# Performance work log

Measured on AMD Instinct MI355X. Metric: run time of the kernel, lower is better.

Reference implementation:

```python
import jax, jax.numpy as jnp
import numpy as np
from jax import lax

FS, DW, CIN, COUT, NCLS, BATCH = 128, 8, 64, 256, 2, 512
K1, S1 = FS // 4, FS // 8          # 32, 16
L = FS * DW                        # 1024
T = (L - K1) // S1 + 1             # 63 SNN timesteps
BN_EPS = 1e-5


@jax.custom_vjp
def spike(u):
    """Heaviside spike on (v - threshold); surrogate grad exp(-|u|) (tau_grad=scale_grad=1)."""
    return (u >= 0).astype(u.dtype)

def _spike_fwd(u):
    return (u >= 0).astype(u.dtype), u

def _spike_bwd(u, g):
    return (g * jnp.exp(-jnp.abs(u)),)

spike.defvjp(_spike_fwd, _spike_bwd)


def cuba(x, threshold, current_decay, voltage_decay):
    """CUBA LIF scan. x: [N,C,T] -> binary spikes [N,C,T].
    i[t] = (1-cd)*i[t-1] + x[t]; v[t] = (1-vd)*v[t-1] + i[t]; s = v>=theta; v *= (1-s)."""
    cd, vd = 1.0 - current_decay, 1.0 - voltage_decay
    xs = jnp.moveaxis(x, -1, 0)  # [T,N,C]
    zero = jnp.zeros(x.shape[:-1], x.dtype)

    def step(carry, xt):
        i, v = carry
        i = cd * i + xt
        v = vd * v + i
        s = spike(v - threshold)
        v = v * (1.0 - s)
        return (i, v), s

    _, s = lax.scan(step, (zero, zero), xs)
    return jnp.moveaxis(s, 0, -1)


def conv1d(x, w, b, stride, pad):
    y = lax.conv_general_dilated(x, w, (stride,), [(pad, pad)],
                                 dimension_numbers=('NCH', 'OIH', 'NCH'))
    return y + b[None, :, None]


def bn(x, g, b, m, v):
    scale = g / jnp.sqrt(v + BN_EPS)
    return (x - m[None, :, None]) * scale[None, :, None] + b[None, :, None]


def setup_inputs() -> dict:
    key = jax.random.key(0)
    ks = jax.random.split(key, 12)
    return {
        'x':       jax.random.normal(ks[0], (BATCH, CIN, L), jnp.float32),
        'conv1_w': jax.random.normal(ks[1], (COUT, CIN, K1), jnp.float32) * 0.05,
        'conv1_b': jax.random.normal(ks[2], (COUT,), jnp.float32) * 0.05,
        'bn1_g':   jax.random.uniform(ks[3], (COUT,), jnp.float32, 0.5, 1.5),
        'bn1_b':   jax.random.normal(ks[4], (COUT,), jnp.float32) * 0.1,
        'bn1_m':   jax.random.normal(ks[5], (COUT,), jnp.float32) * 0.1,
        'bn1_v':   jax.random.uniform(ks[6], (COUT,), jnp.float32, 0.5, 1.5),
        'conv2_w': jax.random.normal(ks[7], (COUT, COUT, 3), jnp.float32) * 0.05,
        'conv2_b': jax.random.normal(ks[8], (COUT,), jnp.float32) * 0.05,
        'bn2_g':   jax.random.uniform(ks[9], (COUT,), jnp.float32, 0.5, 1.5),
        'bn2_b':   jax.random.normal(ks[10], (COUT,), jnp.float32) * 0.1,
        'bn2_m':   jax.random.normal(ks[11], (COUT,), jnp.float32) * 0.1,
        'bn2_v':   jax.random.uniform(jax.random.fold_in(key, 100), (COUT,), jnp.float32, 0.5, 1.5),
        'w1':      jax.random.normal(jax.random.fold_in(key, 101), (COUT, COUT), jnp.float32) * 0.1,
        'w2':      jax.random.normal(jax.random.fold_in(key, 102), (NCLS, COUT), jnp.float32) * 0.1,
    }


def reference(x, conv1_w, conv1_b, bn1_g, bn1_b, bn1_m, bn1_v,
              conv2_w, conv2_b, bn2_g, bn2_b, bn2_m, bn2_v, w1, w2):
    # CNN frontend (eval mode: BN uses running stats, dropout is identity)
    z = bn(conv1d(x, conv1_w, conv1_b, S1, 0), bn1_g, bn1_b, bn1_m, bn1_v)   # [N,COUT,T]
    z = bn(conv1d(z, conv2_w, conv2_b, 1, 1), bn2_g, bn2_b, bn2_m, bn2_v)    # [N,COUT,T]
    # CUBA Input encoder block: threshold=0.3, current_decay=0.9, voltage_decay=0.9
    z = cuba(z, 0.3, 0.9, 0.9)
    # CUBA Dense blocks (bias-free synapse per timestep + LIF): threshold=0.1, cd=1, vd=0.1
    z = cuba(jnp.einsum('oc,nct->not', w1, z), 0.1, 1.0, 0.1)
    z = cuba(jnp.einsum('oc,nct->not', w2, z), 0.1, 1.0, 0.1)
    return z  # binary spike trains [N, n_classes, T]
```

## Files before the change

### kernel.cpp

```cpp
#include <hip/hip_runtime.h>
#include <cstdint>
#include <cstddef>


typedef _Float16 half8 __attribute__((ext_vector_type(8)));
typedef float floatx4 __attribute__((ext_vector_type(4)));

__device__ __forceinline__ void split_f32(float v, _Float16& hi, _Float16& lo) {
    _Float16 h = (_Float16)v;
    hi = h;
    lo = (_Float16)((v - (float)h) * 2048.0f);
}

typedef const __attribute__((address_space(1))) unsigned int* gas_ptr;
typedef __attribute__((address_space(3))) unsigned int* las_ptr;
__device__ __forceinline__ void lds_dma16(const void* g, void* l) {
    __builtin_amdgcn_global_load_lds((gas_ptr)g, (las_ptr)l, 16, 0, 0);
}

__global__ __launch_bounds__(256) void prep_kernel(
    const float* __restrict__ c1w, const float* __restrict__ c1b,
    const float* __restrict__ g1,  const float* __restrict__ b1,
    const float* __restrict__ m1,  const float* __restrict__ v1,
    const float* __restrict__ c2w, const float* __restrict__ c2b,
    const float* __restrict__ g2,  const float* __restrict__ b2,
    const float* __restrict__ m2,  const float* __restrict__ v2,
    const float* __restrict__ w1,
    _Float16* __restrict__ w1h, _Float16* __restrict__ w1l,
    _Float16* __restrict__ w2h, _Float16* __restrict__ w2l,
    _Float16* __restrict__ wdh, _Float16* __restrict__ wdl,
    float* __restrict__ ab1, float* __restrict__ ab2)
{
    const int id = blockIdx.x * 256 + threadIdx.x;
    if (id < 256) {
        float a1 = g1[id] / sqrtf(v1[id] + 1e-5f);
        ab1[id]       = a1;
        ab1[256 + id] = (c1b[id] - m1[id]) * a1 + b1[id];
        float a2 = g2[id] / sqrtf(v2[id] + 1e-5f);
        ab2[id]       = a2;
        ab2[256 + id] = (c2b[id] - m2[id]) * a2 + b2[id];
    }
    split_f32(w1[id], wdh[id], wdl[id]);
    for (int idx = id; idx < 256 * 2048; idx += 65536)
        split_f32(c1w[idx], w1h[idx], w1l[idx]);
    for (int idx = id; idx < 256 * 768; idx += 65536) {
        const int o  = idx / 768;
        const int r  = idx - o * 768;
        const int dt = r >> 8;
        const int c  = r & 255;
        split_f32(c2w[o * 768 + c * 3 + dt], w2h[idx], w2l[idx]);
    }
}

__global__ __launch_bounds__(256, 2) void conv1_mfma(
    const float* __restrict__ x,
    const _Float16* __restrict__ w1h, const _Float16* __restrict__ w1l,
    const float* __restrict__ ab,
    _Float16* __restrict__ z1h, _Float16* __restrict__ z1l)
{
    __shared__ _Float16 Ah[2][4][128][8];
    __shared__ _Float16 Al[2][4][128][8];
    __shared__ _Float16 Bh[2][4][128][8];
    __shared__ _Float16 Bl[2][4][128][8];

    const int tid = threadIdx.x;
    const int bm = blockIdx.x, bn = blockIdx.y;
    const int lr = tid & 127;
    const int h  = tid >> 7;

    const int am = bm * 128 + lr;
    const int an = am / 63, at = am - an * 63;
    const float* arow = x + (size_t)an * 65536 + at * 16 + h * 16;

    const int lane = tid & 63;
    const int wv   = tid >> 6;
    const int mw   = wv & 1, nw = wv >> 1;
    const int quad = lane >> 4;
    const int l15  = lane & 15;

    const int q0 = wv >> 1;
    const int rh = (wv & 1) * 64;
    const _Float16* bh_g = w1h + (size_t)(bn * 128 + rh + lane) * 2048;
    const _Float16* bl_g = w1l + (size_t)(bn * 128 + rh + lane) * 2048;

    floatx4 accA[4][4] = {};
    floatx4 accB[4][4] = {};

    union U { _Float16 hf[8]; int4 v; };
    float va[16];

    {
        *(float4*)&va[0]  = *(const float4*)(arow);
        *(float4*)&va[4]  = *(const float4*)(arow + 4);
        *(float4*)&va[8]  = *(const float4*)(arow + 8);
        *(float4*)&va[12] = *(const float4*)(arow + 12);
        lds_dma16(bh_g + q0 * 8,       &Bh[0][q0    ][rh][0]);
        lds_dma16(bh_g + (q0 + 2) * 8, &Bh[0][q0 + 2][rh][0]);
        lds_dma16(bl_g + q0 * 8,       &Bl[0][q0    ][rh][0]);
        lds_dma16(bl_g + (q0 + 2) * 8, &Bl[0][q0 + 2][rh][0]);
        U c0h, c0l, c1h, c1l;
#pragma unroll
        for (int j = 0; j < 8; ++j) split_f32(va[j],     c0h.hf[j], c0l.hf[j]);
#pragma unroll
        for (int j = 0; j < 8; ++j) split_f32(va[8 + j], c1h.hf[j], c1l.hf[j]);
        *(int4*)&Ah[0][2*h  ][lr][0] = c0h.v;
        *(int4*)&Ah[0][2*h+1][lr][0] = c1h.v;
        *(int4*)&Al[0][2*h  ][lr][0] = c0l.v;
        *(int4*)&Al[0][2*h+1][lr][0] = c1l.v;
        __syncthreads();
    }

    int cur = 0;
    for (int it = 0; it < 64; ++it) {
        const int nxt = cur ^ 1;
        const bool pf = (it < 63);

        if (pf) {
            const float* ap = arow + (it + 1) * 1024;
            *(float4*)&va[0]  = *(const float4*)(ap);
            *(float4*)&va[4]  = *(const float4*)(ap + 4);
            *(float4*)&va[8]  = *(const float4*)(ap + 8);
            *(float4*)&va[12] = *(const float4*)(ap + 12);
            const int ko = (it + 1) * 32;
            lds_dma16(bh_g + ko + q0 * 8,       &Bh[nxt][q0    ][rh][0]);
            lds_dma16(bh_g + ko + (q0 + 2) * 8, &Bh[nxt][q0 + 2][rh][0]);
            lds_dma16(bl_g + ko + q0 * 8,       &Bl[nxt][q0    ][rh][0]);
            lds_dma16(bl_g + ko + (q0 + 2) * 8, &Bl[nxt][q0 + 2][rh][0]);
        }

        half8 fah[4], fal[4], fbh[4], fbl[4];
#pragma unroll
        for (int t = 0; t < 4; ++t) {
            fah[t] = *(const half8*)&Ah[cur][quad][mw*64 + t*16 + l15][0];
            fal[t] = *(const half8*)&Al[cur][quad][mw*64 + t*16 + l15][0];
            fbh[t] = *(const half8*)&Bh[cur][quad][nw*64 + t*16 + l15][0];
            fbl[t] = *(const half8*)&Bl[cur][quad][nw*64 + t*16 + l15][0];
        }
#pragma unroll
        for (int ti = 0; ti < 4; ++ti)
#pragma unroll
            for (int tj = 0; tj < 4; ++tj) {
                accA[ti][tj] = __builtin_amdgcn_mfma_f32_16x16x32_f16(fah[ti], fbh[tj], accA[ti][tj], 0, 0, 0);
                accB[ti][tj] = __builtin_amdgcn_mfma_f32_16x16x32_f16(fah[ti], fbl[tj], accB[ti][tj], 0, 0, 0);
                accB[ti][tj] = __builtin_amdgcn_mfma_f32_16x16x32_f16(fal[ti], fbh[tj], accB[ti][tj], 0, 0, 0);
            }

        if (pf) {
            U c0h, c0l, c1h, c1l;
#pragma unroll
            for (int j = 0; j < 8; ++j) split_f32(va[j],     c0h.hf[j], c0l.hf[j]);
#pragma unroll
            for (int j = 0; j < 8; ++j) split_f32(va[8 + j], c1h.hf[j], c1l.hf[j]);
            *(int4*)&Ah[nxt][2*h  ][lr][0] = c0h.v;
            *(int4*)&Ah[nxt][2*h+1][lr][0] = c1h.v;
            *(int4*)&Al[nxt][2*h  ][lr][0] = c0l.v;
            *(int4*)&Al[nxt][2*h+1][lr][0] = c1l.v;
        }
        __syncthreads();
        cur = nxt;
    }

#pragma unroll
    for (int tj = 0; tj < 4; ++tj) {
        const int o = bn*128 + nw*64 + tj*16 + l15;
        const float alpha = ab[o], beta = ab[256 + o];
#pragma unroll
        for (int ti = 0; ti < 4; ++ti) {
            const int m0 = bm*128 + mw*64 + ti*16 + quad*4;
#pragma unroll
            for (int r = 0; r < 4; ++r) {
                float c = accA[ti][tj][r] + accB[ti][tj][r] * (1.0f/2048.0f);
                float z = c * alpha + beta;
                _Float16 zh, zl;
                split_f32(z, zh, zl);
                const size_t off = (size_t)(m0 + r) * 256 + o;
                z1h[off] = zh;
                z1l[off] = zl;
            }
        }
    }
}

__global__ __launch_bounds__(256, 2) void conv2_mfma(
    const _Float16* __restrict__ z1h, const _Float16* __restrict__ z1l,
    const _Float16* __restrict__ w2h, const _Float16* __restrict__ w2l,
    const float* __restrict__ ab, float* __restrict__ z2)
{
    __shared__ _Float16 Ah[2][4][128][8];
    __shared__ _Float16 Al[2][4][128][8];
    __shared__ _Float16 Bh[2][4][128][8];
    __shared__ _Float16 Bl[2][4][128][8];

    const int tid = threadIdx.x;
    const int bm = blockIdx.x, bn = blockIdx.y;
    const int lr = tid & 127;
    const int h  = tid >> 7;

    const int am = bm * 128 + lr;
    const int an = am / 63, at = am - an * 63;
    const _Float16* abase_h = z1h + (size_t)an * 16128;
    const _Float16* abase_l = z1l + (size_t)an * 16128;

    const int lane = tid & 63;
    const int wv   = tid >> 6;
    const int mw   = wv & 1, nw = wv >> 1;
    const int quad = lane >> 4;
    const int l15  = lane & 15;

    const int q0 = wv >> 1;
    const int rh = (wv & 1) * 64;
    const _Float16* bh_g = w2h + (size_t)(bn * 128 + rh + lane) * 768;
    const _Float16* bl_g = w2l + (size_t)(bn * 128 + rh + lane) * 768;

    floatx4 accA[4][4] = {};
    floatx4 accB[4][4] = {};

    const int4 z4 = {0, 0, 0, 0};
    int4 a0h, a1h, a0l, a1l;

    auto loadA = [&](int it, int4& r0h, int4& r1h, int4& r0l, int4& r1l) {
        const int kap0 = it * 32;
        const int dt   = kap0 >> 8;
        const int c0   = kap0 & 255;
        const int trow = at + dt - 1;
        const bool valid = (trow >= 0) && (trow < 63);
        const _Float16* aph = abase_h + trow * 256 + c0 + h * 16;
        const _Float16* apl = abase_l + trow * 256 + c0 + h * 16;
        r0h = valid ? *(const int4*)(aph)     : z4;
        r1h = valid ? *(const int4*)(aph + 8) : z4;
        r0l = valid ? *(const int4*)(apl)     : z4;
        r1l = valid ? *(const int4*)(apl + 8) : z4;
    };

    {
        loadA(0, a0h, a1h, a0l, a1l);
        lds_dma16(bh_g + q0 * 8,       &Bh[0][q0    ][rh][0]);
        lds_dma16(bh_g + (q0 + 2) * 8, &Bh[0][q0 + 2][rh][0]);
        lds_dma16(bl_g + q0 * 8,       &Bl[0][q0    ][rh][0]);
        lds_dma16(bl_g + (q0 + 2) * 8, &Bl[0][q0 + 2][rh][0]);
        *(int4*)&Ah[0][2*h  ][lr][0] = a0h;
        *(int4*)&Ah[0][2*h+1][lr][0] = a1h;
        *(int4*)&Al[0][2*h  ][lr][0] = a0l;
        *(int4*)&Al[0][2*h+1][lr][0] = a1l;
        __syncthreads();
    }

    int cur = 0;
    for (int it = 0; it < 24; ++it) {
        const int nxt = cur ^ 1;
        const bool pf = (it < 23);

        if (pf) {
            loadA(it + 1, a0h, a1h, a0l, a1l);
            const int ko = (it + 1) * 32;
            lds_dma16(bh_g + ko + q0 * 8,       &Bh[nxt][q0    ][rh][0]);
            lds_dma16(bh_g + ko + (q0 + 2) * 8, &Bh[nxt][q0 + 2][rh][0]);
            lds_dma16(bl_g + ko + q0 * 8,       &Bl[nxt][q0    ][rh][0]);
            lds_dma16(bl_g + ko + (q0 + 2) * 8, &Bl[nxt][q0 + 2][rh][0]);
        }

        half8 fah[4], fal[4], fbh[4], fbl[4];
#pragma unroll
        for (int t = 0; t < 4; ++t) {
            fah[t] = *(const half8*)&Ah[cur][quad][mw*64 + t*16 + l15][0];
            fal[t] = *(const half8*)&Al[cur][quad][mw*64 + t*16 + l15][0];
            fbh[t] = *(const half8*)&Bh[cur][quad][nw*64 + t*16 + l15][0];
            fbl[t] = *(const half8*)&Bl[cur][quad][nw*64 + t*16 + l15][0];
        }
#pragma unroll
        for (int ti = 0; ti < 4; ++ti)
#pragma unroll
            for (int tj = 0; tj < 4; ++tj) {
                accA[ti][tj] = __builtin_amdgcn_mfma_f32_16x16x32_f16(fah[ti], fbh[tj], accA[ti][tj], 0, 0, 0);
                accB[ti][tj] = __builtin_amdgcn_mfma_f32_16x16x32_f16(fah[ti], fbl[tj], accB[ti][tj], 0, 0, 0);
                accB[ti][tj] = __builtin_amdgcn_mfma_f32_16x16x32_f16(fal[ti], fbh[tj], accB[ti][tj], 0, 0, 0);
            }

        if (pf) {
            *(int4*)&Ah[nxt][2*h  ][lr][0] = a0h;
            *(int4*)&Ah[nxt][2*h+1][lr][0] = a1h;
            *(int4*)&Al[nxt][2*h  ][lr][0] = a0l;
            *(int4*)&Al[nxt][2*h+1][lr][0] = a1l;
        }
        __syncthreads();
        cur = nxt;
    }

#pragma unroll
    for (int tj = 0; tj < 4; ++tj) {
        const int o = bn*128 + nw*64 + tj*16 + l15;
        const float alpha = ab[o], beta = ab[256 + o];
#pragma unroll
        for (int ti = 0; ti < 4; ++ti) {
            const int m0 = bm*128 + mw*64 + ti*16 + quad*4;
#pragma unroll
            for (int r = 0; r < 4; ++r) {
                float c = accA[ti][tj][r] + accB[ti][tj][r] * (1.0f/2048.0f);
                z2[(size_t)(m0 + r) * 256 + o] = c * alpha + beta;
            }
        }
    }
}

__global__ __launch_bounds__(256) void cuba1_kernel(
    const float* __restrict__ z2, _Float16* __restrict__ s1)
{
    const int n   = blockIdx.x;
    const int tid = threadIdx.x;
    const float* zrow = z2 + (size_t)n * 16128 + tid;
    _Float16*    srow = s1 + (size_t)n * 16128 + tid;
    float cur = 0.f, vol = 0.f;
    for (int t = 0; t < 63; ++t) {
        float xv = zrow[(size_t)t * 256];
        cur = 0.1f * cur + xv;
        vol = 0.1f * vol + cur;
        bool sp = (vol - 0.3f) >= 0.f;
        srow[(size_t)t * 256] = sp ? (_Float16)1.0f : (_Float16)0.0f;
        if (sp) vol = 0.f;
    }
}

__global__ __launch_bounds__(256, 2) void dense1_mfma(
    const _Float16* __restrict__ s1,
    const _Float16* __restrict__ wdh, const _Float16* __restrict__ wdl,
    float* __restrict__ y1)
{
    __shared__ _Float16 As[2][4][128][8];
    __shared__ _Float16 Bh[2][4][128][8];
    __shared__ _Float16 Bl[2][4][128][8];

    const int tid = threadIdx.x;
    const int bm = blockIdx.x, bn = blockIdx.y;

    const int lane = tid & 63;
    const int wv   = tid >> 6;
    const int mw   = wv & 1, nw = wv >> 1;
    const int quad = lane >> 4;
    const int l15  = lane & 15;

    const int q0 = wv >> 1;
    const int rh = (wv & 1) * 64;
    const _Float16* a_g  = s1  + (size_t)(bm * 128 + rh + lane) * 256;
    const _Float16* bh_g = wdh + (size_t)(bn * 128 + rh + lane) * 256;
    const _Float16* bl_g = wdl + (size_t)(bn * 128 + rh + lane) * 256;

    floatx4 accA[4][4] = {};
    floatx4 accB[4][4] = {};

    {
        lds_dma16(a_g  + q0 * 8,       &As[0][q0    ][rh][0]);
        lds_dma16(a_g  + (q0 + 2) * 8, &As[0][q0 + 2][rh][0]);
        lds_dma16(bh_g + q0 * 8,       &Bh[0][q0    ][rh][0]);
        lds_dma16(bh_g + (q0 + 2) * 8, &Bh[0][q0 + 2][rh][0]);
        lds_dma16(bl_g + q0 * 8,       &Bl[0][q0    ][rh][0]);
        lds_dma16(bl_g + (q0 + 2) * 8, &Bl[0][q0 + 2][rh][0]);
        __syncthreads();
    }

    int cur = 0;
    for (int it = 0; it < 8; ++it) {
        const int nxt = cur ^ 1;
        const bool pf = (it < 7);

        if (pf) {
            const int ko = (it + 1) * 32;
            lds_dma16(a_g  + ko + q0 * 8,       &As[nxt][q0    ][rh][0]);
            lds_dma16(a_g  + ko + (q0 + 2) * 8, &As[nxt][q0 + 2][rh][0]);
            lds_dma16(bh_g + ko + q0 * 8,       &Bh[nxt][q0    ][rh][0]);
            lds_dma16(bh_g + ko + (q0 + 2) * 8, &Bh[nxt][q0 + 2][rh][0]);
            lds_dma16(bl_g + ko + q0 * 8,       &Bl[nxt][q0    ][rh][0]);
            lds_dma16(bl_g + ko + (q0 + 2) * 8, &Bl[nxt][q0 + 2][rh][0]);
        }

        half8 fa[4], fbh[4], fbl[4];
#pragma unroll
        for (int t = 0; t < 4; ++t) {
            fa[t]  = *(const half8*)&As[cur][quad][mw*64 + t*16 + l15][0];
            fbh[t] = *(const half8*)&Bh[cur][quad][nw*64 + t*16 + l15][0];
            fbl[t] = *(const half8*)&Bl[cur][quad][nw*64 + t*16 + l15][0];
        }
#pragma unroll
        for (int ti = 0; ti < 4; ++ti)
#pragma unroll
            for (int tj = 0; tj < 4; ++tj) {
                accA[ti][tj] = __builtin_amdgcn_mfma_f32_16x16x32_f16(fa[ti], fbh[tj], accA[ti][tj], 0, 0, 0);
                accB[ti][tj] = __builtin_amdgcn_mfma_f32_16x16x32_f16(fa[ti], fbl[tj], accB[ti][tj], 0, 0, 0);
            }

        __syncthreads();
        cur = nxt;
    }

#pragma unroll
    for (int tj = 0; tj < 4; ++tj) {
        const int o = bn*128 + nw*64 + tj*16 + l15;
#pragma unroll
        for (int ti = 0; ti < 4; ++ti) {
            const int m0 = bm*128 + mw*64 + ti*16 + quad*4;
#pragma unroll
            for (int r = 0; r < 4; ++r)
                y1[(size_t)(m0 + r) * 256 + o] =
                    accA[ti][tj][r] + accB[ti][tj][r] * (1.0f/2048.0f);
        }
    }
}

__global__ __launch_bounds__(256) void snn_tail(
    const float* __restrict__ y1, const float* __restrict__ w2,
    float* __restrict__ out)
{
    __shared__ unsigned long long M2[256];
    __shared__ float Y[2 * 63];
    const int n   = blockIdx.x;
    const int tid = threadIdx.x;

    {
        const float* yrow = y1 + (size_t)n * 16128 + tid;
        float v = 0.f;
        unsigned long long mask2 = 0ull;
        for (int t = 0; t < 63; ++t) {
            float yv = yrow[(size_t)t * 256];
            v = 0.9f * v + yv;
            if ((v - 0.1f) >= 0.f) { mask2 |= (1ull << t); v = 0.f; }
        }
        M2[tid] = mask2;
    }
    __syncthreads();

    if (tid < 126) {
        const int cls = tid / 63;
        const int t   = tid - cls * 63;
        const float* wrow = w2 + cls * 256;
        float acc = 0.f;
#pragma unroll 4
        for (int o = 0; o < 256; ++o)
            acc += ((M2[o] >> t) & 1ull) ? wrow[o] : 0.f;
        Y[cls * 63 + t] = acc;
    }
    __syncthreads();
    if (tid < 2) {
        float v = 0.f;
        float* orow = out + (size_t)n * 126 + tid * 63;
        for (int t = 0; t < 63; ++t) {
            v = 0.9f * v + Y[tid * 63 + t];
            float u = v - 0.1f;
            float s = (u >= 0.f) ? 1.f : 0.f;
            orow[t] = s;
            v = (u >= 0.f) ? 0.f : v;
        }
    }
}

extern "C" void kernel_launch(void* const* d_in, const int* in_sizes, int n_in,
                              void* d_out, int out_size, void* d_ws, size_t ws_size,
                              hipStream_t stream)
{
    const float* x    = (const float*)d_in[0];
    const float* c1w  = (const float*)d_in[1];
    const float* c1b  = (const float*)d_in[2];
    const float* g1   = (const float*)d_in[3];
    const float* b1   = (const float*)d_in[4];
    const float* m1   = (const float*)d_in[5];
    const float* v1   = (const float*)d_in[6];
    const float* c2w  = (const float*)d_in[7];
    const float* c2b  = (const float*)d_in[8];
    const float* g2   = (const float*)d_in[9];
    const float* b2   = (const float*)d_in[10];
    const float* m2   = (const float*)d_in[11];
    const float* v2   = (const float*)d_in[12];
    const float* w1   = (const float*)d_in[13];
    const float* w2   = (const float*)d_in[14];
    float* out = (float*)d_out;

    float* ws = (float*)d_ws;
    float*    zA  = ws;
    _Float16* z1h = (_Float16*)zA;
    _Float16* z1l = (_Float16*)(zA + 4128768);
    float*    y1  = zA;
    float*    z2  = zA + 8257536;
    _Float16* s1  = (_Float16*)(z2 + 8257536);
    float*    wsp = z2 + 8257536 + 4128768;
    _Float16* w1h = (_Float16*)wsp;
    _Float16* w1l = (_Float16*)(wsp + 262144);
    _Float16* w2h = (_Float16*)(wsp + 2*262144);
    _Float16* w2l = (_Float16*)(wsp + 2*262144 + 98304);
    _Float16* wdh = (_Float16*)(wsp + 2*262144 + 2*98304);
    _Float16* wdl = (_Float16*)(wsp + 2*262144 + 2*98304 + 32768);
    float*    ab1 = wsp + 2*262144 + 2*98304 + 2*32768;
    float*    ab2 = ab1 + 512;

    prep_kernel<<<256, 256, 0, stream>>>(c1w, c1b, g1, b1, m1, v1,
                                         c2w, c2b, g2, b2, m2, v2,
                                         w1, w1h, w1l, w2h, w2l, wdh, wdl,
                                         ab1, ab2);
    conv1_mfma<<<dim3(252, 2), 256, 0, stream>>>(x, w1h, w1l, ab1, z1h, z1l);
    conv2_mfma<<<dim3(252, 2), 256, 0, stream>>>(z1h, z1l, w2h, w2l, ab2, z2);
    cuba1_kernel<<<512, 256, 0, stream>>>(z2, s1);
    dense1_mfma<<<dim3(252, 2), 256, 0, stream>>>(s1, wdh, wdl, y1);
    snn_tail<<<512, 256, 0, stream>>>(y1, w2, out);
}
```

Before: 449.7 us.

## Deepen prefetch pipelines with partial vmcnt barriers in conv and dense GEMMs

```diff
diff --git a/kernel.cpp b/kernel.cpp
--- a/kernel.cpp
+++ b/kernel.cpp
@@ -17,6 +17,8 @@
 __device__ __forceinline__ void lds_dma16(const void* g, void* l) {
     __builtin_amdgcn_global_load_lds((gas_ptr)g, (las_ptr)l, 16, 0, 0);
 }
+
+#define BARRIER_VM(N) asm volatile("s_waitcnt vmcnt(" #N ") lgkmcnt(0)\n\ts_barrier" ::: "memory")
 
 __global__ __launch_bounds__(256) void prep_kernel(
     const float* __restrict__ c1w, const float* __restrict__ c1b,
@@ -87,46 +89,53 @@
     floatx4 accB[4][4] = {};
 
     union U { _Float16 hf[8]; int4 v; };
-    float va[16];
+    float va0[16], va1[16];
 
     {
-        *(float4*)&va[0]  = *(const float4*)(arow);
-        *(float4*)&va[4]  = *(const float4*)(arow + 4);
-        *(float4*)&va[8]  = *(const float4*)(arow + 8);
-        *(float4*)&va[12] = *(const float4*)(arow + 12);
         lds_dma16(bh_g + q0 * 8,       &Bh[0][q0    ][rh][0]);
         lds_dma16(bh_g + (q0 + 2) * 8, &Bh[0][q0 + 2][rh][0]);
         lds_dma16(bl_g + q0 * 8,       &Bl[0][q0    ][rh][0]);
         lds_dma16(bl_g + (q0 + 2) * 8, &Bl[0][q0 + 2][rh][0]);
+        __builtin_amdgcn_sched_barrier(0);
+        *(float4*)&va0[0]  = *(const float4*)(arow);
+        *(float4*)&va0[4]  = *(const float4*)(arow + 4);
+        *(float4*)&va0[8]  = *(const float4*)(arow + 8);
+        *(float4*)&va0[12] = *(const float4*)(arow + 12);
+        const float* ap1 = arow + 1024;
+        *(float4*)&va1[0]  = *(const float4*)(ap1);
+        *(float4*)&va1[4]  = *(const float4*)(ap1 + 4);
+        *(float4*)&va1[8]  = *(const float4*)(ap1 + 8);
+        *(float4*)&va1[12] = *(const float4*)(ap1 + 12);
         U c0h, c0l, c1h, c1l;
 #pragma unroll
-        for (int j = 0; j < 8; ++j) split_f32(va[j],     c0h.hf[j], c0l.hf[j]);
-#pragma unroll
-        for (int j = 0; j < 8; ++j) split_f32(va[8 + j], c1h.hf[j], c1l.hf[j]);
+        for (int j = 0; j < 8; ++j) split_f32(va0[j],     c0h.hf[j], c0l.hf[j]);
+#pragma unroll
+        for (int j = 0; j < 8; ++j) split_f32(va0[8 + j], c1h.hf[j], c1l.hf[j]);
         *(int4*)&Ah[0][2*h  ][lr][0] = c0h.v;
         *(int4*)&Ah[0][2*h+1][lr][0] = c1h.v;
         *(int4*)&Al[0][2*h  ][lr][0] = c0l.v;
         *(int4*)&Al[0][2*h+1][lr][0] = c1l.v;
-        __syncthreads();
-    }
-
-    int cur = 0;
-    for (int it = 0; it < 64; ++it) {
+        BARRIER_VM(4);
+    }
+
+    auto body = [&](int it, float (&vaC)[16], float (&vaN)[16], int cur) {
         const int nxt = cur ^ 1;
-        const bool pf = (it < 63);
-
-        if (pf) {
-            const float* ap = arow + (it + 1) * 1024;
-            *(float4*)&va[0]  = *(const float4*)(ap);
-            *(float4*)&va[4]  = *(const float4*)(ap + 4);
-            *(float4*)&va[8]  = *(const float4*)(ap + 8);
-            *(float4*)&va[12] = *(const float4*)(ap + 12);
+        if (it + 1 < 64) {
             const int ko = (it + 1) * 32;
             lds_dma16(bh_g + ko + q0 * 8,       &Bh[nxt][q0    ][rh][0]);
             lds_dma16(bh_g + ko + (q0 + 2) * 8, &Bh[nxt][q0 + 2][rh][0]);
             lds_dma16(bl_g + ko + q0 * 8,       &Bl[nxt][q0    ][rh][0]);
             lds_dma16(bl_g + ko + (q0 + 2) * 8, &Bl[nxt][q0 + 2][rh][0]);
         }
+        __builtin_amdgcn_sched_barrier(0);
+        if (it + 2 < 64) {
+            const float* ap = arow + (it + 2) * 1024;
+            *(float4*)&vaC[0]  = *(const float4*)(ap);
+            *(float4*)&vaC[4]  = *(const float4*)(ap + 4);
+            *(float4*)&vaC[8]  = *(const float4*)(ap + 8);
+            *(float4*)&vaC[12] = *(const float4*)(ap + 12);
+        }
+        __builtin_amdgcn_sched_barrier(0);
 
         half8 fah[4], fal[4], fbh[4], fbl[4];
 #pragma unroll
@@ -145,19 +154,24 @@
                 accB[ti][tj] = __builtin_amdgcn_mfma_f32_16x16x32_f16(fal[ti], fbh[tj], accB[ti][tj], 0, 0, 0);
             }
 
-        if (pf) {
+        if (it + 1 < 64) {
             U c0h, c0l, c1h, c1l;
 #pragma unroll
-            for (int j = 0; j < 8; ++j) split_f32(va[j],     c0h.hf[j], c0l.hf[j]);
-#pragma unroll
-            for (int j = 0; j < 8; ++j) split_f32(va[8 + j], c1h.hf[j], c1l.hf[j]);
+            for (int j = 0; j < 8; ++j) split_f32(vaN[j],     c0h.hf[j], c0l.hf[j]);
+#pragma unroll
+            for (int j = 0; j < 8; ++j) split_f32(vaN[8 + j], c1h.hf[j], c1l.hf[j]);
             *(int4*)&Ah[nxt][2*h  ][lr][0] = c0h.v;
             *(int4*)&Ah[nxt][2*h+1][lr][0] = c1h.v;
             *(int4*)&Al[nxt][2*h  ][lr][0] = c0l.v;
             *(int4*)&Al[nxt][2*h+1][lr][0] = c1l.v;
         }
-        __syncthreads();
-        cur = nxt;
+        if (it + 2 < 64)      { BARRIER_VM(4); }
+        else if (it + 1 < 64) { BARRIER_VM(0); }
+    };
+
+    for (int it = 0; it < 64; it += 2) {
+        body(it,     va0, va1, 0);
+        body(it + 1, va1, va0, 1);
     }
 
 #pragma unroll
@@ -216,48 +230,51 @@
     floatx4 accB[4][4] = {};
 
     const int4 z4 = {0, 0, 0, 0};
-    int4 a0h, a1h, a0l, a1l;
-
-    auto loadA = [&](int it, int4& r0h, int4& r1h, int4& r0l, int4& r1l) {
+    int4 wA0[4], wA1[4];
+    bool v0, v1;
+
+    auto issueA = [&](int it, int4 (&w)[4], bool& valid) {
         const int kap0 = it * 32;
         const int dt   = kap0 >> 8;
         const int c0   = kap0 & 255;
         const int trow = at + dt - 1;
-        const bool valid = (trow >= 0) && (trow < 63);
-        const _Float16* aph = abase_h + trow * 256 + c0 + h * 16;
-        const _Float16* apl = abase_l + trow * 256 + c0 + h * 16;
-        r0h = valid ? *(const int4*)(aph)     : z4;
-        r1h = valid ? *(const int4*)(aph + 8) : z4;
-        r0l = valid ? *(const int4*)(apl)     : z4;
-        r1l = valid ? *(const int4*)(apl + 8) : z4;
+        valid = (trow >= 0) && (trow < 63);
+        const int trc  = trow < 0 ? 0 : (trow > 62 ? 62 : trow);
+        const _Float16* aph = abase_h + trc * 256 + c0 + h * 16;
+        const _Float16* apl = abase_l + trc * 256 + c0 + h * 16;
+        w[0] = *(const int4*)(aph);
+        w[1] = *(const int4*)(aph + 8);
+        w[2] = *(const int4*)(apl);
+        w[3] = *(const int4*)(apl + 8);
     };
 
     {
-        loadA(0, a0h, a1h, a0l, a1l);
         lds_dma16(bh_g + q0 * 8,       &Bh[0][q0    ][rh][0]);
         lds_dma16(bh_g + (q0 + 2) * 8, &Bh[0][q0 + 2][rh][0]);
         lds_dma16(bl_g + q0 * 8,       &Bl[0][q0    ][rh][0]);
         lds_dma16(bl_g + (q0 + 2) * 8, &Bl[0][q0 + 2][rh][0]);
-        *(int4*)&Ah[0][2*h  ][lr][0] = a0h;
-        *(int4*)&Ah[0][2*h+1][lr][0] = a1h;
-        *(int4*)&Al[0][2*h  ][lr][0] = a0l;
-        *(int4*)&Al[0][2*h+1][lr][0] = a1l;
-        __syncthreads();
-    }
-
-    int cur = 0;
-    for (int it = 0; it < 24; ++it) {
+        __builtin_amdgcn_sched_barrier(0);
+        issueA(0, wA0, v0);
+        issueA(1, wA1, v1);
+        *(int4*)&Ah[0][2*h  ][lr][0] = v0 ? wA0[0] : z4;
+        *(int4*)&Ah[0][2*h+1][lr][0] = v0 ? wA0[1] : z4;
+        *(int4*)&Al[0][2*h  ][lr][0] = v0 ? wA0[2] : z4;
+        *(int4*)&Al[0][2*h+1][lr][0] = v0 ? wA0[3] : z4;
+        BARRIER_VM(4);
+    }
+
+    auto body = [&](int it, int4 (&wC)[4], bool& vC, int4 (&wN)[4], bool& vN, int cur) {
         const int nxt = cur ^ 1;
-        const bool pf = (it < 23);
-
-        if (pf) {
-            loadA(it + 1, a0h, a1h, a0l, a1l);
+        if (it + 1 < 24) {
             const int ko = (it + 1) * 32;
             lds_dma16(bh_g + ko + q0 * 8,       &Bh[nxt][q0    ][rh][0]);
             lds_dma16(bh_g + ko + (q0 + 2) * 8, &Bh[nxt][q0 + 2][rh][0]);
             lds_dma16(bl_g + ko + q0 * 8,       &Bl[nxt][q0    ][rh][0]);
             lds_dma16(bl_g + ko + (q0 + 2) * 8, &Bl[nxt][q0 + 2][rh][0]);
         }
+        __builtin_amdgcn_sched_barrier(0);
+        if (it + 2 < 24) issueA(it + 2, wC, vC);
+        __builtin_amdgcn_sched_barrier(0);
 
         half8 fah[4], fal[4], fbh[4], fbl[4];
 #pragma unroll
@@ -276,14 +293,19 @@
                 accB[ti][tj] = __builtin_amdgcn_mfma_f32_16x16x32_f16(fal[ti], fbh[tj], accB[ti][tj], 0, 0, 0);
             }
 
-        if (pf) {
-            *(int4*)&Ah[nxt][2*h  ][lr][0] = a0h;
-            *(int4*)&Ah[nxt][2*h+1][lr][0] = a1h;
-            *(int4*)&Al[nxt][2*h  ][lr][0] = a0l;
-            *(int4*)&Al[nxt][2*h+1][lr][0] = a1l;
-        }
-        __syncthreads();
-        cur = nxt;
+        if (it + 1 < 24) {
+            *(int4*)&Ah[nxt][2*h  ][lr][0] = vN ? wN[0] : z4;
+            *(int4*)&Ah[nxt][2*h+1][lr][0] = vN ? wN[1] : z4;
+            *(int4*)&Al[nxt][2*h  ][lr][0] = vN ? wN[2] : z4;
+            *(int4*)&Al[nxt][2*h+1][lr][0] = vN ? wN[3] : z4;
+        }
+        if (it + 2 < 24)      { BARRIER_VM(4); }
+        else if (it + 1 < 24) { BARRIER_VM(0); }
+    };
+
+    for (int it = 0; it < 24; it += 2) {
+        body(it,     wA0, v0, wA1, v1, 0);
+        body(it + 1, wA1, v1, wA0, v0, 1);
     }
 
 #pragma unroll
@@ -310,13 +332,19 @@
     const float* zrow = z2 + (size_t)n * 16128 + tid;
     _Float16*    srow = s1 + (size_t)n * 16128 + tid;
     float cur = 0.f, vol = 0.f;
-    for (int t = 0; t < 63; ++t) {
-        float xv = zrow[(size_t)t * 256];
-        cur = 0.1f * cur + xv;
-        vol = 0.1f * vol + cur;
-        bool sp = (vol - 0.3f) >= 0.f;
-        srow[(size_t)t * 256] = sp ? (_Float16)1.0f : (_Float16)0.0f;
-        if (sp) vol = 0.f;
+    for (int tb = 0; tb < 63; tb += 9) {
+        float xv[9];
+#pragma unroll
+        for (int j = 0; j < 9; ++j)
+            xv[j] = zrow[(size_t)(tb + j) * 256];
+#pragma unroll
+        for (int j = 0; j < 9; ++j) {
+            cur = 0.1f * cur + xv[j];
+            vol = 0.1f * vol + cur;
+            bool sp = (vol - 0.3f) >= 0.f;
+            srow[(size_t)(tb + j) * 256] = sp ? (_Float16)1.0f : (_Float16)0.0f;
+            if (sp) vol = 0.f;
+        }
     }
 }
 
@@ -325,9 +353,9 @@
     const _Float16* __restrict__ wdh, const _Float16* __restrict__ wdl,
     float* __restrict__ y1)
 {
-    __shared__ _Float16 As[2][4][128][8];
-    __shared__ _Float16 Bh[2][4][128][8];
-    __shared__ _Float16 Bl[2][4][128][8];
+    __shared__ _Float16 As[3][4][128][8];
+    __shared__ _Float16 Bh[3][4][128][8];
+    __shared__ _Float16 Bl[3][4][128][8];
 
     const int tid = threadIdx.x;
     const int bm = blockIdx.x, bn = blockIdx.y;
@@ -347,37 +375,31 @@
     floatx4 accA[4][4] = {};
     floatx4 accB[4][4] = {};
 
-    {
-        lds_dma16(a_g  + q0 * 8,       &As[0][q0    ][rh][0]);
-        lds_dma16(a_g  + (q0 + 2) * 8, &As[0][q0 + 2][rh][0]);
-        lds_dma16(bh_g + q0 * 8,       &Bh[0][q0    ][rh][0]);
-        lds_dma16(bh_g + (q0 + 2) * 8, &Bh[0][q0 + 2][rh][0]);
-        lds_dma16(bl_g + q0 * 8,       &Bl[0][q0    ][rh][0]);
-        lds_dma16(bl_g + (q0 + 2) * 8, &Bl[0][q0 + 2][rh][0]);
-        __syncthreads();
-    }
-
-    int cur = 0;
+    auto stage = [&](int it, int b) {
+        const int ko = it * 32;
+        lds_dma16(a_g  + ko + q0 * 8,       &As[b][q0    ][rh][0]);
+        lds_dma16(a_g  + ko + (q0 + 2) * 8, &As[b][q0 + 2][rh][0]);
+        lds_dma16(bh_g + ko + q0 * 8,       &Bh[b][q0    ][rh][0]);
+        lds_dma16(bh_g + ko + (q0 + 2) * 8, &Bh[b][q0 + 2][rh][0]);
+        lds_dma16(bl_g + ko + q0 * 8,       &Bl[b][q0    ][rh][0]);
+        lds_dma16(bl_g + ko + (q0 + 2) * 8, &Bl[b][q0 + 2][rh][0]);
+    };
+
+    stage(0, 0);
+    stage(1, 1);
+    BARRIER_VM(6);
+
+#pragma unroll
     for (int it = 0; it < 8; ++it) {
-        const int nxt = cur ^ 1;
-        const bool pf = (it < 7);
-
-        if (pf) {
-            const int ko = (it + 1) * 32;
-            lds_dma16(a_g  + ko + q0 * 8,       &As[nxt][q0    ][rh][0]);
-            lds_dma16(a_g  + ko + (q0 + 2) * 8, &As[nxt][q0 + 2][rh][0]);
-            lds_dma16(bh_g + ko + q0 * 8,       &Bh[nxt][q0    ][rh][0]);
-            lds_dma16(bh_g + ko + (q0 + 2) * 8, &Bh[nxt][q0 + 2][rh][0]);
-            lds_dma16(bl_g + ko + q0 * 8,       &Bl[nxt][q0    ][rh][0]);
-            lds_dma16(bl_g + ko + (q0 + 2) * 8, &Bl[nxt][q0 + 2][rh][0]);
-        }
+        const int b = it % 3;
+        if (it + 2 < 8) stage(it + 2, (it + 2) % 3);
 
         half8 fa[4], fbh[4], fbl[4];
 #pragma unroll
         for (int t = 0; t < 4; ++t) {
-            fa[t]  = *(const half8*)&As[cur][quad][mw*64 + t*16 + l15][0];
-            fbh[t] = *(const half8*)&Bh[cur][quad][nw*64 + t*16 + l15][0];
-            fbl[t] = *(const half8*)&Bl[cur][quad][nw*64 + t*16 + l15][0];
+            fa[t]  = *(const half8*)&As[b][quad][mw*64 + t*16 + l15][0];
+            fbh[t] = *(const half8*)&Bh[b][quad][nw*64 + t*16 + l15][0];
+            fbl[t] = *(const half8*)&Bl[b][quad][nw*64 + t*16 + l15][0];
         }
 #pragma unroll
         for (int ti = 0; ti < 4; ++ti)
@@ -387,8 +409,8 @@
                 accB[ti][tj] = __builtin_amdgcn_mfma_f32_16x16x32_f16(fa[ti], fbl[tj], accB[ti][tj], 0, 0, 0);
             }
 
-        __syncthreads();
-        cur = nxt;
+        if (it + 2 < 8)      { BARRIER_VM(6); }
+        else if (it + 1 < 8) { BARRIER_VM(0); }
     }
 
 #pragma unroll
```

After: 479.0 us. 1.07x slower.
